# Kernel tuning notes

Measured on AMD Instinct MI355X. Metric: run time of the kernel, lower is better.

Reference implementation:

```python
import jax, jax.numpy as jnp
import numpy as np


def setup_inputs() -> dict:
    key = jax.random.key(0)
    k1, k2, k3 = jax.random.split(key, 3)
    B, N, D, A = 64, 500000, 512, 7
    batch_rep = jax.random.normal(k1, (B, D), dtype=jnp.float32)
    representations = jax.random.normal(k2, (N, D), dtype=jnp.float32)
    actions = jax.random.normal(k3, (N, A), dtype=jnp.float32)
    return {
        "batch_rep": batch_rep,
        "representations": representations,
        "actions": actions,
        "k": 16,
    }


def reference(batch_rep, representations, actions, k):
    # torch.cdist (p=2): pairwise Euclidean distances [B, N] via the
    d2 = (
        jnp.sum(batch_rep * batch_rep, axis=1, keepdims=True)
        - 2.0 * (batch_rep @ representations.T)
        + jnp.sum(representations * representations, axis=1)[None, :]
    )
    dist = jnp.sqrt(jnp.maximum(d2, 0.0))  # [B, N]

    # torch.topk(largest=False): smallest-k distances == top-k of negated.
    neg_top, indices = jax.lax.top_k(-dist, k)  # [B, k]
    top_k_dist = -neg_top

    # weights = softmax(-dist) over the k neighbors
    weights = jax.nn.softmax(-top_k_dist, axis=1)  # [B, k]

    top_k_actions = actions[indices]  # gather -> [B, k, A]
    pred = jnp.sum(top_k_actions * weights[..., None], axis=1)  # [B, A]
    return pred, indices
```

## Files before the change

### kernel.cpp

```cpp
#include <hip/hip_runtime.h>
#include <stdint.h>

typedef _Float16 f16;
typedef _Float16 f16x8 __attribute__((ext_vector_type(8)));
typedef float f32x4 __attribute__((ext_vector_type(4)));

#define INF_F __builtin_inff()
#define KM 24

__device__ __forceinline__ bool lexLess(float s1, int n1, float s2, int n2) {
    return (s1 < s2) || (s1 == s2 && n1 < n2);
}

__global__ __launch_bounds__(256) void prepack_kernel(
    const float* __restrict__ brep, uint4* __restrict__ xfrag)
{
    const int e = blockIdx.x * 256 + threadIdx.x;
    if (e >= 4096) return;
    const int ms = e & 3;
    const int lane = (e >> 2) & 63;
    const int ks = e >> 8;
    const int m = ms * 16 + (lane & 15);
    const int k = ks * 32 + (lane >> 4) * 8;
    const float* src = brep + m * 512 + k;
    unsigned short hb[8];
    #pragma unroll
    for (int j = 0; j < 8; j++) {
        f16 v = (f16)src[j];
        hb[j] = __builtin_bit_cast(unsigned short, v);
    }
    uint4 o;
    o.x = (unsigned)hb[0] | ((unsigned)hb[1] << 16);
    o.y = (unsigned)hb[2] | ((unsigned)hb[3] << 16);
    o.z = (unsigned)hb[4] | ((unsigned)hb[5] << 16);
    o.w = (unsigned)hb[6] | ((unsigned)hb[7] << 16);
    xfrag[e] = o;
}

__global__ __launch_bounds__(256, 3) void dist_topk_kernel(
    const float* __restrict__ reps, const uint4* __restrict__ xfrag,
    float* __restrict__ cs, int* __restrict__ ci,
    int N, int tilesBase, int tilesRem)
{
    __shared__ __align__(16) float slds[64][68];
    __shared__ float topd[16][64];
    __shared__ int   topi[16][64];

    const int tid = threadIdx.x;
    const int w = tid >> 6, lane = tid & 63;
    const int li = lane & 15, q = lane >> 4;
    const int b = blockIdx.x;
    const int t0 = b * tilesBase + min(b, tilesRem);
    const int tcount = tilesBase + (b < tilesRem ? 1 : 0);

    float thr = INF_F; int thrn = 0x7fffffff; int cnt = 0;

    for (int ti = 0; ti < tcount; ti++) {
        const int n0 = (t0 + ti) * 64;
        const int row = n0 + 16 * w + li;
        const size_t rowc = (size_t)(row < N ? row : N - 1);
        const float* bp = reps + rowc * 512 + q * 8;

        f32x4 acc0 = {0.f,0.f,0.f,0.f}, acc1 = {0.f,0.f,0.f,0.f};
        f32x4 acc2 = {0.f,0.f,0.f,0.f}, acc3 = {0.f,0.f,0.f,0.f};
        float ynacc = 0.f;

        #pragma unroll 2
        for (int ks = 0; ks < 16; ks++) {
            const float4 y0 = *(const float4*)(bp + ks * 32);
            const float4 y1 = *(const float4*)(bp + ks * 32 + 4);
            const uint4* ap = xfrag + (((size_t)ks * 64 + lane) << 2);
            const uint4 a0u = ap[0];
            const uint4 a1u = ap[1];
            const uint4 a2u = ap[2];
            const uint4 a3u = ap[3];
            ynacc = fmaf(y0.x, y0.x, fmaf(y0.y, y0.y, fmaf(y0.z, y0.z, fmaf(y0.w, y0.w, ynacc))));
            ynacc = fmaf(y1.x, y1.x, fmaf(y1.y, y1.y, fmaf(y1.z, y1.z, fmaf(y1.w, y1.w, ynacc))));
            const auto p0 = __builtin_amdgcn_cvt_pkrtz(y0.x, y0.y);
            const auto p1 = __builtin_amdgcn_cvt_pkrtz(y0.z, y0.w);
            const auto p2 = __builtin_amdgcn_cvt_pkrtz(y1.x, y1.y);
            const auto p3 = __builtin_amdgcn_cvt_pkrtz(y1.z, y1.w);
            uint4 bu;
            bu.x = __builtin_bit_cast(unsigned, p0);
            bu.y = __builtin_bit_cast(unsigned, p1);
            bu.z = __builtin_bit_cast(unsigned, p2);
            bu.w = __builtin_bit_cast(unsigned, p3);
            const f16x8 bf = __builtin_bit_cast(f16x8, bu);
            acc0 = __builtin_amdgcn_mfma_f32_16x16x32_f16(__builtin_bit_cast(f16x8, a0u), bf, acc0, 0, 0, 0);
            acc1 = __builtin_amdgcn_mfma_f32_16x16x32_f16(__builtin_bit_cast(f16x8, a1u), bf, acc1, 0, 0, 0);
            acc2 = __builtin_amdgcn_mfma_f32_16x16x32_f16(__builtin_bit_cast(f16x8, a2u), bf, acc2, 0, 0, 0);
            acc3 = __builtin_amdgcn_mfma_f32_16x16x32_f16(__builtin_bit_cast(f16x8, a3u), bf, acc3, 0, 0, 0);
        }
        ynacc += __shfl_xor(ynacc, 16);
        ynacc += __shfl_xor(ynacc, 32);
        const float yn = (row < N) ? ynacc : INF_F;

        __syncthreads();

        {
            const int nl = 16 * w + li;
            float4 sv;
            sv.x = fmaf(-2.f, acc0[0], yn); sv.y = fmaf(-2.f, acc0[1], yn);
            sv.z = fmaf(-2.f, acc0[2], yn); sv.w = fmaf(-2.f, acc0[3], yn);
            *(float4*)(&slds[nl][0  + 4 * q]) = sv;
            sv.x = fmaf(-2.f, acc1[0], yn); sv.y = fmaf(-2.f, acc1[1], yn);
            sv.z = fmaf(-2.f, acc1[2], yn); sv.w = fmaf(-2.f, acc1[3], yn);
            *(float4*)(&slds[nl][16 + 4 * q]) = sv;
            sv.x = fmaf(-2.f, acc2[0], yn); sv.y = fmaf(-2.f, acc2[1], yn);
            sv.z = fmaf(-2.f, acc2[2], yn); sv.w = fmaf(-2.f, acc2[3], yn);
            *(float4*)(&slds[nl][32 + 4 * q]) = sv;
            sv.x = fmaf(-2.f, acc3[0], yn); sv.y = fmaf(-2.f, acc3[1], yn);
            sv.z = fmaf(-2.f, acc3[2], yn); sv.w = fmaf(-2.f, acc3[3], yn);
            *(float4*)(&slds[nl][48 + 4 * q]) = sv;
        }
        __syncthreads();

        if (tid < 64) {
            const int r = tid;
            #pragma unroll 4
            for (int j = 0; j < 64; j++) {
                const float s = slds[j][r];
                const int n = n0 + j;
                if (lexLess(s, n, thr, thrn)) {
                    if (cnt < 16) {
                        topd[cnt][r] = s; topi[cnt][r] = n; cnt++;
                        if (cnt == 16) {
                            float tv = topd[0][r]; int tn = topi[0][r];
                            #pragma unroll
                            for (int u = 1; u < 16; u++) {
                                float v = topd[u][r]; int nn = topi[u][r];
                                if (!lexLess(v, nn, tv, tn)) { tv = v; tn = nn; }
                            }
                            thr = tv; thrn = tn;
                        }
                    } else {
                        #pragma unroll
                        for (int u = 0; u < 16; u++)
                            if (topd[u][r] == thr && topi[u][r] == thrn) {
                                topd[u][r] = s; topi[u][r] = n; break;
                            }
                        float tv = topd[0][r]; int tn = topi[0][r];
                        #pragma unroll
                        for (int u = 1; u < 16; u++) {
                            float v = topd[u][r]; int nn = topi[u][r];
                            if (!lexLess(v, nn, tv, tn)) { tv = v; tn = nn; }
                        }
                        thr = tv; thrn = tn;
                    }
                }
            }
        }
    }

    if (tid < 64) {
        const size_t base = ((size_t)b * 64 + tid) * 16;
        for (int j = 0; j < 16; j++) {
            cs[base + j] = (j < cnt) ? topd[j][tid] : INF_F;
            ci[base + j] = (j < cnt) ? topi[j][tid] : 0x7fffffff;
        }
    }
}

__global__ __launch_bounds__(256) void merge_kernel(
    const float* __restrict__ cs, const int* __restrict__ ci,
    const float* __restrict__ brep, const float* __restrict__ reps,
    const float* __restrict__ acts,
    float* __restrict__ out, int NBLK, int N, int BA)
{
    const int r = blockIdx.x;
    const int tid = threadIdx.x;
    __shared__ __align__(16) float xrow[512];
    __shared__ float S1s[256 * KM];
    __shared__ int   S1i[256 * KM];
    __shared__ float S2s[32 * KM];
    __shared__ int   S2i[32 * KM];
    __shared__ double fd[KM];
    __shared__ int    fn[KM];

    if (tid < 128)
        *(float4*)(&xrow[tid * 4]) = *(const float4*)(&brep[(size_t)r * 512 + tid * 4]);

    float ls[KM]; int li[KM];
    #pragma unroll
    for (int j = 0; j < KM; j++) { ls[j] = INF_F; li[j] = 0x7fffffff; }
    float mv = INF_F; int mn = 0x7fffffff; int mp = 0;
    const int total = NBLK * 16;
    for (int e = tid; e < total; e += 256) {
        const int blk = e >> 4, j = e & 15;
        const size_t a = (size_t)blk * 1024 + (size_t)r * 16 + j;
        const float s = cs[a]; const int n = ci[a];
        if (lexLess(s, n, mv, mn)) {
            ls[mp] = s; li[mp] = n;
            mv = ls[0]; mn = li[0]; mp = 0;
            #pragma unroll
            for (int u = 1; u < KM; u++)
                if (!lexLess(ls[u], li[u], mv, mn)) { mv = ls[u]; mn = li[u]; mp = u; }
        }
    }
    #pragma unroll
    for (int j = 0; j < KM; j++) { S1s[tid * KM + j] = ls[j]; S1i[tid * KM + j] = li[j]; }
    __syncthreads();

    if (tid < 32) {
        #pragma unroll
        for (int j = 0; j < KM; j++) { ls[j] = INF_F; li[j] = 0x7fffffff; }
        mv = INF_F; mn = 0x7fffffff; mp = 0;
        for (int e = tid * 8 * KM; e < (tid * 8 + 8) * KM; e++) {
            const float s = S1s[e]; const int n = S1i[e];
            if (lexLess(s, n, mv, mn)) {
                ls[mp] = s; li[mp] = n;
                mv = ls[0]; mn = li[0]; mp = 0;
                #pragma unroll
                for (int u = 1; u < KM; u++)
                    if (!lexLess(ls[u], li[u], mv, mn)) { mv = ls[u]; mn = li[u]; mp = u; }
            }
        }
        #pragma unroll
        for (int j = 0; j < KM; j++) { S2s[tid * KM + j] = ls[j]; S2i[tid * KM + j] = li[j]; }
    }
    __syncthreads();

    if (tid == 0) {
        #pragma unroll
        for (int j = 0; j < KM; j++) { ls[j] = INF_F; li[j] = 0x7fffffff; }
        mv = INF_F; mn = 0x7fffffff; mp = 0;
        for (int e = 0; e < 32 * KM; e++) {
            const float s = S2s[e]; const int n = S2i[e];
            if (lexLess(s, n, mv, mn)) {
                ls[mp] = s; li[mp] = n;
                mv = ls[0]; mn = li[0]; mp = 0;
                #pragma unroll
                for (int u = 1; u < KM; u++)
                    if (!lexLess(ls[u], li[u], mv, mn)) { mv = ls[u]; mn = li[u]; mp = u; }
            }
        }
        for (int j = 0; j < KM; j++) fn[j] = li[j];
    }
    __syncthreads();

    if (tid < KM) {
        const int n = fn[tid];
        double d = 1.0e300;
        if (n >= 0 && n < N) {
            d = 0.0;
            const float* yp = reps + (size_t)n * 512;
            for (int i = 0; i < 512; i += 4) {
                float4 yv = *(const float4*)(yp + i);
                double d0 = (double)xrow[i + 0] - (double)yv.x;
                double d1 = (double)xrow[i + 1] - (double)yv.y;
                double d2 = (double)xrow[i + 2] - (double)yv.z;
                double d3 = (double)xrow[i + 3] - (double)yv.w;
                d += d0 * d0 + d1 * d1 + d2 * d2 + d3 * d3;
            }
        }
        fd[tid] = d;
    }
    __syncthreads();

    if (tid == 0) {
        int ord[KM];
        for (int j = 0; j < KM; j++) ord[j] = j;
        for (int a = 0; a < 16; a++) {
            int best = a;
            for (int u = a + 1; u < KM; u++) {
                const int ou = ord[u], ob = ord[best];
                if (fd[ou] < fd[ob] || (fd[ou] == fd[ob] && fn[ou] < fn[ob])) best = u;
            }
            int tmp = ord[a]; ord[a] = ord[best]; ord[best] = tmp;
        }
        double dist[16];
        for (int j = 0; j < 16; j++) {
            double v = fd[ord[j]];
            dist[j] = sqrt(v > 0.0 ? v : 0.0);
        }
        double wv[16], wsum = 0.0;
        for (int j = 0; j < 16; j++) { wv[j] = exp(dist[0] - dist[j]); wsum += wv[j]; }
        for (int a = 0; a < 7; a++) {
            double s = 0.0;
            for (int j = 0; j < 16; j++)
                s += wv[j] * (double)acts[(size_t)fn[ord[j]] * 7 + a];
            out[r * 7 + a] = (float)(s / wsum);
        }
        for (int j = 0; j < 16; j++)
            out[BA + r * 16 + j] = (float)fn[ord[j]];
    }
}

extern "C" void kernel_launch(void* const* d_in, const int* in_sizes, int n_in,
                              void* d_out, int out_size, void* d_ws, size_t ws_size,
                              hipStream_t stream) {
    const float* brep = (const float*)d_in[0];
    const float* reps = (const float*)d_in[1];
    const float* acts = (const float*)d_in[2];
    const int D = 512;
    const int B = in_sizes[0] / D;
    const int N = in_sizes[1] / D;
    float* out = (float*)d_out;

    int NBLK = 1536;
    const size_t perblk = (size_t)64 * 16 * 8;
    if ((size_t)NBLK * perblk + 65536 > ws_size)
        NBLK = (int)((ws_size - 65536) / perblk);
    if (NBLK < 1) NBLK = 1;

    float* cs = (float*)d_ws;
    int* ci = (int*)((char*)d_ws + (size_t)NBLK * 64 * 16 * 4);
    uint4* xfrag = (uint4*)((char*)d_ws + (size_t)NBLK * perblk);

    const int TT = (N + 63) / 64;
    const int tilesBase = TT / NBLK;
    const int tilesRem = TT % NBLK;

    prepack_kernel<<<16, 256, 0, stream>>>(brep, xfrag);
    dist_topk_kernel<<<NBLK, 256, 0, stream>>>(reps, xfrag, cs, ci, N, tilesBase, tilesRem);
    merge_kernel<<<B, 256, 0, stream>>>(cs, ci, brep, reps, acts, out, NBLK, N, B * 7);
}
```

Measured before the change: 1.553 ms.

## Stage query fragments in LDS, double rows per block, prefetch rep rows

After: 2.679 ms. +72.5%, slower.

```diff
diff --git a/kernel.cpp b/kernel.cpp
--- a/kernel.cpp
+++ b/kernel.cpp
@@ -11,14 +11,19 @@
 __device__ __forceinline__ bool lexLess(float s1, int n1, float s2, int n2) {
     return (s1 < s2) || (s1 == s2 && n1 < n2);
 }
+
+#define GLOAD_LDS16(gsrc, ldst)                                                  \
+    __builtin_amdgcn_global_load_lds(                                            \
+        (const __attribute__((address_space(1))) uint32_t*)(gsrc),               \
+        (__attribute__((address_space(3))) uint32_t*)(ldst), 16, 0, 0)
 
 __global__ __launch_bounds__(256) void prepack_kernel(
     const float* __restrict__ brep, uint4* __restrict__ xfrag)
 {
     const int e = blockIdx.x * 256 + threadIdx.x;
     if (e >= 4096) return;
-    const int ms = e & 3;
-    const int lane = (e >> 2) & 63;
+    const int lane = e & 63;
+    const int ms = (e >> 6) & 3;
     const int ks = e >> 8;
     const int m = ms * 16 + (lane & 15);
     const int k = ks * 32 + (lane >> 4) * 8;
@@ -37,12 +42,13 @@
     xfrag[e] = o;
 }
 
-__global__ __launch_bounds__(256, 3) void dist_topk_kernel(
+__global__ __launch_bounds__(512, 2) void dist_topk_kernel(
     const float* __restrict__ reps, const uint4* __restrict__ xfrag,
     float* __restrict__ cs, int* __restrict__ ci,
     int N, int tilesBase, int tilesRem)
 {
-    __shared__ __align__(16) float slds[64][68];
+    __shared__ uint4 afr[4096];
+    __shared__ __align__(16) float slds[128][68];
     __shared__ float topd[16][64];
     __shared__ int   topi[16][64];
 
@@ -53,27 +59,34 @@
     const int t0 = b * tilesBase + min(b, tilesRem);
     const int tcount = tilesBase + (b < tilesRem ? 1 : 0);
 
+    #pragma unroll
+    for (int i = 0; i < 8; i++) {
+        const int base = i * 512 + w * 64;
+        GLOAD_LDS16(xfrag + base + lane, (char*)afr + (size_t)base * 16);
+    }
+    __syncthreads();
+
     float thr = INF_F; int thrn = 0x7fffffff; int cnt = 0;
 
     for (int ti = 0; ti < tcount; ti++) {
-        const int n0 = (t0 + ti) * 64;
+        const int n0 = (t0 + ti) * 128;
         const int row = n0 + 16 * w + li;
         const size_t rowc = (size_t)(row < N ? row : N - 1);
         const float* bp = reps + rowc * 512 + q * 8;
 
+        float4 yv[32];
+        #pragma unroll
+        for (int i = 0; i < 32; i++)
+            yv[i] = *(const float4*)(bp + (i >> 1) * 32 + (i & 1) * 4);
+
         f32x4 acc0 = {0.f,0.f,0.f,0.f}, acc1 = {0.f,0.f,0.f,0.f};
         f32x4 acc2 = {0.f,0.f,0.f,0.f}, acc3 = {0.f,0.f,0.f,0.f};
         float ynacc = 0.f;
 
-        #pragma unroll 2
+        #pragma unroll
         for (int ks = 0; ks < 16; ks++) {
-            const float4 y0 = *(const float4*)(bp + ks * 32);
-            const float4 y1 = *(const float4*)(bp + ks * 32 + 4);
-            const uint4* ap = xfrag + (((size_t)ks * 64 + lane) << 2);
-            const uint4 a0u = ap[0];
-            const uint4 a1u = ap[1];
-            const uint4 a2u = ap[2];
-            const uint4 a3u = ap[3];
+            const float4 y0 = yv[2 * ks];
+            const float4 y1 = yv[2 * ks + 1];
             ynacc = fmaf(y0.x, y0.x, fmaf(y0.y, y0.y, fmaf(y0.z, y0.z, fmaf(y0.w, y0.w, ynacc))));
             ynacc = fmaf(y1.x, y1.x, fmaf(y1.y, y1.y, fmaf(y1.z, y1.z, fmaf(y1.w, y1.w, ynacc))));
             const auto p0 = __builtin_amdgcn_cvt_pkrtz(y0.x, y0.y);
@@ -86,6 +99,10 @@
             bu.z = __builtin_bit_cast(unsigned, p2);
             bu.w = __builtin_bit_cast(unsigned, p3);
             const f16x8 bf = __builtin_bit_cast(f16x8, bu);
+            const uint4 a0u = afr[(ks * 4 + 0) * 64 + lane];
+            const uint4 a1u = afr[(ks * 4 + 1) * 64 + lane];
+            const uint4 a2u = afr[(ks * 4 + 2) * 64 + lane];
+            const uint4 a3u = afr[(ks * 4 + 3) * 64 + lane];
             acc0 = __builtin_amdgcn_mfma_f32_16x16x32_f16(__builtin_bit_cast(f16x8, a0u), bf, acc0, 0, 0, 0);
             acc1 = __builtin_amdgcn_mfma_f32_16x16x32_f16(__builtin_bit_cast(f16x8, a1u), bf, acc1, 0, 0, 0);
             acc2 = __builtin_amdgcn_mfma_f32_16x16x32_f16(__builtin_bit_cast(f16x8, a2u), bf, acc2, 0, 0, 0);
@@ -117,8 +134,8 @@
 
         if (tid < 64) {
             const int r = tid;
-            #pragma unroll 4
-            for (int j = 0; j < 64; j++) {
+            #pragma unroll 2
+            for (int j = 0; j < 128; j++) {
                 const float s = slds[j][r];
                 const int n = n0 + j;
                 if (lexLess(s, n, thr, thrn)) {
@@ -297,7 +314,7 @@
     const int N = in_sizes[1] / D;
     float* out = (float*)d_out;
 
-    int NBLK = 1536;
+    int NBLK = 512;
     const size_t perblk = (size_t)64 * 16 * 8;
     if ((size_t)NBLK * perblk + 65536 > ws_size)
         NBLK = (int)((ws_size - 65536) / perblk);
@@ -307,11 +324,11 @@
     int* ci = (int*)((char*)d_ws + (size_t)NBLK * 64 * 16 * 4);
     uint4* xfrag = (uint4*)((char*)d_ws + (size_t)NBLK * perblk);
 
-    const int TT = (N + 63) / 64;
+    const int TT = (N + 127) / 128;
     const int tilesBase = TT / NBLK;
     const int tilesRem = TT % NBLK;
 
     prepack_kernel<<<16, 256, 0, stream>>>(brep, xfrag);
-    dist_topk_kernel<<<NBLK, 256, 0, stream>>>(reps, xfrag, cs, ci, N, tilesBase, tilesRem);
+    dist_topk_kernel<<<NBLK, 512, 0, stream>>>(reps, xfrag, cs, ci, N, tilesBase, tilesRem);
     merge_kernel<<<B, 256, 0, stream>>>(cs, ci, brep, reps, acts, out, NBLK, N, B * 7);
 }
```

## Rotate top-k scan across waves, prefetch GEMM operands, coalesce A fragments

Applied to the files above, without the earlier changes.

After: 1.529 ms. Within noise of the previous version (-1.6%).

```diff
diff --git a/kernel.cpp b/kernel.cpp
--- a/kernel.cpp
+++ b/kernel.cpp
@@ -17,8 +17,8 @@
 {
     const int e = blockIdx.x * 256 + threadIdx.x;
     if (e >= 4096) return;
-    const int ms = e & 3;
-    const int lane = (e >> 2) & 63;
+    const int lane = e & 63;
+    const int ms = (e >> 6) & 3;
     const int ks = e >> 8;
     const int m = ms * 16 + (lane & 15);
     const int k = ks * 32 + (lane >> 4) * 8;
@@ -37,7 +37,7 @@
     xfrag[e] = o;
 }
 
-__global__ __launch_bounds__(256, 3) void dist_topk_kernel(
+__global__ __launch_bounds__(256, 4) void dist_topk_kernel(
     const float* __restrict__ reps, const uint4* __restrict__ xfrag,
     float* __restrict__ cs, int* __restrict__ ci,
     int N, int tilesBase, int tilesRem)
@@ -45,6 +45,9 @@
     __shared__ __align__(16) float slds[64][68];
     __shared__ float topd[16][64];
     __shared__ int   topi[16][64];
+    __shared__ float thrS[64];
+    __shared__ int   thrnS[64];
+    __shared__ int   cntS[64];
 
     const int tid = threadIdx.x;
     const int w = tid >> 6, lane = tid & 63;
@@ -53,7 +56,8 @@
     const int t0 = b * tilesBase + min(b, tilesRem);
     const int tcount = tilesBase + (b < tilesRem ? 1 : 0);
 
-    float thr = INF_F; int thrn = 0x7fffffff; int cnt = 0;
+    if (tid < 64) { thrS[tid] = INF_F; thrnS[tid] = 0x7fffffff; cntS[tid] = 0; }
+    __syncthreads();
 
     for (int ti = 0; ti < tcount; ti++) {
         const int n0 = (t0 + ti) * 64;
@@ -65,32 +69,47 @@
         f32x4 acc2 = {0.f,0.f,0.f,0.f}, acc3 = {0.f,0.f,0.f,0.f};
         float ynacc = 0.f;
 
-        #pragma unroll 2
+        float4 yA0 = *(const float4*)(bp);
+        float4 yA1 = *(const float4*)(bp + 4);
+        uint4 aA0 = xfrag[(0 * 4 + 0) * 64 + lane];
+        uint4 aA1 = xfrag[(0 * 4 + 1) * 64 + lane];
+        uint4 aA2 = xfrag[(0 * 4 + 2) * 64 + lane];
+        uint4 aA3 = xfrag[(0 * 4 + 3) * 64 + lane];
+
+        #pragma unroll
         for (int ks = 0; ks < 16; ks++) {
-            const float4 y0 = *(const float4*)(bp + ks * 32);
-            const float4 y1 = *(const float4*)(bp + ks * 32 + 4);
-            const uint4* ap = xfrag + (((size_t)ks * 64 + lane) << 2);
-            const uint4 a0u = ap[0];
-            const uint4 a1u = ap[1];
-            const uint4 a2u = ap[2];
-            const uint4 a3u = ap[3];
-            ynacc = fmaf(y0.x, y0.x, fmaf(y0.y, y0.y, fmaf(y0.z, y0.z, fmaf(y0.w, y0.w, ynacc))));
-            ynacc = fmaf(y1.x, y1.x, fmaf(y1.y, y1.y, fmaf(y1.z, y1.z, fmaf(y1.w, y1.w, ynacc))));
-            const auto p0 = __builtin_amdgcn_cvt_pkrtz(y0.x, y0.y);
-            const auto p1 = __builtin_amdgcn_cvt_pkrtz(y0.z, y0.w);
-            const auto p2 = __builtin_amdgcn_cvt_pkrtz(y1.x, y1.y);
-            const auto p3 = __builtin_amdgcn_cvt_pkrtz(y1.z, y1.w);
+            float4 yB0, yB1;
+            uint4 aB0, aB1, aB2, aB3;
+            if (ks < 15) {
+                yB0 = *(const float4*)(bp + (ks + 1) * 32);
+                yB1 = *(const float4*)(bp + (ks + 1) * 32 + 4);
+                aB0 = xfrag[((ks + 1) * 4 + 0) * 64 + lane];
+                aB1 = xfrag[((ks + 1) * 4 + 1) * 64 + lane];
+                aB2 = xfrag[((ks + 1) * 4 + 2) * 64 + lane];
+                aB3 = xfrag[((ks + 1) * 4 + 3) * 64 + lane];
+            }
+            ynacc = fmaf(yA0.x, yA0.x, fmaf(yA0.y, yA0.y, fmaf(yA0.z, yA0.z, fmaf(yA0.w, yA0.w, ynacc))));
+            ynacc = fmaf(yA1.x, yA1.x, fmaf(yA1.y, yA1.y, fmaf(yA1.z, yA1.z, fmaf(yA1.w, yA1.w, ynacc))));
+            const auto p0 = __builtin_amdgcn_cvt_pkrtz(yA0.x, yA0.y);
+            const auto p1 = __builtin_amdgcn_cvt_pkrtz(yA0.z, yA0.w);
+            const auto p2 = __builtin_amdgcn_cvt_pkrtz(yA1.x, yA1.y);
+            const auto p3 = __builtin_amdgcn_cvt_pkrtz(yA1.z, yA1.w);
             uint4 bu;
             bu.x = __builtin_bit_cast(unsigned, p0);
             bu.y = __builtin_bit_cast(unsigned, p1);
             bu.z = __builtin_bit_cast(unsigned, p2);
             bu.w = __builtin_bit_cast(unsigned, p3);
             const f16x8 bf = __builtin_bit_cast(f16x8, bu);
-            acc0 = __builtin_amdgcn_mfma_f32_16x16x32_f16(__builtin_bit_cast(f16x8, a0u), bf, acc0, 0, 0, 0);
-            acc1 = __builtin_amdgcn_mfma_f32_16x16x32_f16(__builtin_bit_cast(f16x8, a1u), bf, acc1, 0, 0, 0);
-            acc2 = __builtin_amdgcn_mfma_f32_16x16x32_f16(__builtin_bit_cast(f16x8, a2u), bf, acc2, 0, 0, 0);
-            acc3 = __builtin_amdgcn_mfma_f32_16x16x32_f16(__builtin_bit_cast(f16x8, a3u), bf, acc3, 0, 0, 0);
-        }
+            acc0 = __builtin_amdgcn_mfma_f32_16x16x32_f16(__builtin_bit_cast(f16x8, aA0), bf, acc0, 0, 0, 0);
+            acc1 = __builtin_amdgcn_mfma_f32_16x16x32_f16(__builtin_bit_cast(f16x8, aA1), bf, acc1, 0, 0, 0);
+            acc2 = __builtin_amdgcn_mfma_f32_16x16x32_f16(__builtin_bit_cast(f16x8, aA2), bf, acc2, 0, 0, 0);
+            acc3 = __builtin_amdgcn_mfma_f32_16x16x32_f16(__builtin_bit_cast(f16x8, aA3), bf, acc3, 0, 0, 0);
+            if (ks < 15) {
+                yA0 = yB0; yA1 = yB1;
+                aA0 = aB0; aA1 = aB1; aA2 = aB2; aA3 = aB3;
+            }
+        }
+
         ynacc += __shfl_xor(ynacc, 16);
         ynacc += __shfl_xor(ynacc, 32);
         const float yn = (row < N) ? ynacc : INF_F;
@@ -115,8 +134,9 @@
         }
         __syncthreads();
 
-        if (tid < 64) {
-            const int r = tid;
+        if (w == (ti & 3)) {
+            const int r = lane;
+            float thr = thrS[r]; int thrn = thrnS[r]; int cnt = cntS[r];
             #pragma unroll 4
             for (int j = 0; j < 64; j++) {
                 const float s = slds[j][r];
@@ -149,14 +169,17 @@
                     }
                 }
             }
-        }
-    }
-
+            thrS[r] = thr; thrnS[r] = thrn; cntS[r] = cnt;
+        }
+    }
+
+    __syncthreads();
     if (tid < 64) {
+        const int c = cntS[tid];
         const size_t base = ((size_t)b * 64 + tid) * 16;
         for (int j = 0; j < 16; j++) {
-            cs[base + j] = (j < cnt) ? topd[j][tid] : INF_F;
-            ci[base + j] = (j < cnt) ? topi[j][tid] : 0x7fffffff;
+            cs[base + j] = (j < c) ? topd[j][tid] : INF_F;
+            ci[base + j] = (j < c) ? topi[j][tid] : 0x7fffffff;
         }
     }
 }
@@ -297,7 +320,7 @@
     const int N = in_sizes[1] / D;
     float* out = (float*)d_out;
 
-    int NBLK = 1536;
+    int NBLK = 1024;
     const size_t perblk = (size_t)64 * 16 * 8;
     if ((size_t)NBLK * perblk + 65536 > ws_size)
         NBLK = (int)((ws_size - 65536) / perblk);
```
